# Kernel optimization log

Hardware: AMD Instinct MI355X
Metric: run time of the kernel (lower is better)

## Reference

```python
import jax, jax.numpy as jnp
import numpy as np

B, T, D = 4, 2048, 1024
H = 16            # n_heads
DH = D // H       # head dim
E = 8             # n_micro_experts
DE = 256          # micro_expert_dim
TOP_K = 2
EPS = 1e-5


def _ln(x, g, b):
    m = jnp.mean(x, axis=-1, keepdims=True)
    v = jnp.mean(jnp.square(x - m), axis=-1, keepdims=True)
    return (x - m) * jax.lax.rsqrt(v + EPS) * g + b


def setup_inputs() -> dict:
    key = jax.random.key(0)
    ks = jax.random.split(key, 12)
    s = 0.02
    return {
        "x": jax.random.normal(ks[0], (B, T, D), dtype=jnp.float32),
        "ln1_g": jnp.ones((D,), jnp.float32),
        "ln1_b": jnp.zeros((D,), jnp.float32),
        "in_proj_w": jax.random.normal(ks[1], (3 * D, D), jnp.float32) * s,
        "in_proj_b": jnp.zeros((3 * D,), jnp.float32),
        "out_proj_w": jax.random.normal(ks[2], (D, D), jnp.float32) * s,
        "out_proj_b": jnp.zeros((D,), jnp.float32),
        "ln2_g": jnp.ones((D,), jnp.float32),
        "ln2_b": jnp.zeros((D,), jnp.float32),
        "router_w": jax.random.normal(ks[3], (E, D), jnp.float32) * s,
        "log_temp": jnp.zeros((), jnp.float32),
        "Wg": jax.random.normal(ks[4], (E, DE, D), jnp.float32) * s,  # gate proj per expert
        "Wu": jax.random.normal(ks[5], (E, DE, D), jnp.float32) * s,  # up proj per expert
        "Wd": jax.random.normal(ks[6], (E, D, DE), jnp.float32) * s,  # down proj per expert
    }


def reference(x, ln1_g, ln1_b, in_proj_w, in_proj_b, out_proj_w, out_proj_b,
              ln2_g, ln2_b, router_w, log_temp, Wg, Wu, Wd):
    # --- self-attention block (nn.MultiheadAttention, batch_first, no mask) ---
    h = _ln(x, ln1_g, ln1_b)
    qkv = h @ in_proj_w.T + in_proj_b                       # [B,T,3D]
    q, k, v = jnp.split(qkv, 3, axis=-1)
    q = q.reshape(B, T, H, DH).transpose(0, 2, 1, 3)        # [B,H,T,DH]
    k = k.reshape(B, T, H, DH).transpose(0, 2, 1, 3)
    v = v.reshape(B, T, H, DH).transpose(0, 2, 1, 3)
    scores = jnp.einsum("bhqd,bhkd->bhqk", q, k) / np.sqrt(DH).astype(np.float32)
    attn = jax.nn.softmax(scores, axis=-1)
    o = jnp.einsum("bhqk,bhkd->bhqd", attn, v)              # [B,H,T,DH]
    o = o.transpose(0, 2, 1, 3).reshape(B, T, D)
    x = x + o @ out_proj_w.T + out_proj_b

    # --- MicroExpert MoE (soft top-k via sigmoid suppression, dense experts) ---
    h2 = _ln(x, ln2_g, ln2_b)
    temp = jax.nn.softplus(log_temp) + 0.1
    logits = (h2 @ router_w.T) / temp                       # [B,T,E]
    top_vals, _ = jax.lax.top_k(logits, TOP_K)
    threshold = jax.lax.stop_gradient(top_vals[..., -1:])   # k-th largest, detached
    suppression = jax.nn.sigmoid(10.0 * (logits - threshold))
    weights = jax.nn.softmax(logits * suppression, axis=-1)  # [B,T,E]

    hg = jnp.einsum("btd,efd->btef", h2, Wg)                # [B,T,E,DE]
    hu = jnp.einsum("btd,efd->btef", h2, Wu)
    act = jax.nn.silu(hg) * hu
    out_e = jnp.einsum("btef,edf->bted", act, Wd)           # [B,T,E,D]
    moe = jnp.einsum("bted,bte->btd", out_e, weights)
    return x + moe
```

## Files before the change

### kernel.cpp

```cpp
#include <hip/hip_runtime.h>
#include <hip/hip_bf16.h>
#include <cstddef>
#include <cstdint>

constexpr int Bc  = 4;
constexpr int Tc  = 2048;
constexpr int Dc  = 1024;
constexpr int Hc  = 16;
constexpr int Ec  = 8;
constexpr int DEc = 256;
constexpr int NTOK = Bc * Tc;
constexpr int EDE = Ec * DEc;

typedef __attribute__((ext_vector_type(8)))  short  s8v;
typedef __attribute__((ext_vector_type(4)))  float  f4v;
typedef __attribute__((ext_vector_type(16))) float  f16v;
typedef __attribute__((ext_vector_type(8)))  ushort u8v;
typedef __attribute__((ext_vector_type(4)))  ushort u4v;

constexpr float LOG2E = 1.44269504088896340736f;

__device__ inline ushort f2bf(float f) {
  union { float f; uint32_t u; } v; v.f = f;
  uint32_t r = v.u + 0x7FFFu + ((v.u >> 16) & 1u);
  return (ushort)(r >> 16);
}
__device__ inline float exp2v(float x) {
  float r; asm("v_exp_f32 %0, %1" : "=v"(r) : "v"(x)); return r;
}
__device__ inline float max3f(float a, float b, float c) {
  return fmaxf(fmaxf(a, b), c);
}
__device__ inline float pmax32(float x) {
  float a = x, b = x;
  asm("v_permlane32_swap_b32 %0, %1" : "+v"(b), "+v"(a));
  return fmaxf(a, b);
}
__device__ inline float psum32(float x) {
  float a = x, b = x;
  asm("v_permlane32_swap_b32 %0, %1" : "+v"(b), "+v"(a));
  return a + b;
}

#define GLOAD_LDS(gsrc, ldst)                                        \
  __builtin_amdgcn_global_load_lds(                                  \
      (const __attribute__((address_space(1))) void*)(gsrc),         \
      (__attribute__((address_space(3))) void*)(ldst), 16, 0, 0)

__device__ inline uint32_t cvtpk(float a, float b) {
  uint32_t r;
  asm("v_cvt_pk_bf16_f32 %0, %1, %2" : "=v"(r) : "v"(a), "v"(b));
  return r;
}

__device__ inline u8v pack8(const float4& a, const float4& b) {
  u8v o;
  o[0] = f2bf(a.x); o[1] = f2bf(a.y); o[2] = f2bf(a.z); o[3] = f2bf(a.w);
  o[4] = f2bf(b.x); o[5] = f2bf(b.y); o[6] = f2bf(b.z); o[7] = f2bf(b.w);
  return o;
}

__global__ __launch_bounds__(256)
void convert_all(const float* __restrict__ in_w, const float* __restrict__ out_w,
                 const float* __restrict__ Wg, const float* __restrict__ Wu,
                 const float* __restrict__ Wd,
                 ushort* __restrict__ wb_in, ushort* __restrict__ wb_out,
                 ushort* __restrict__ wb_gu, ushort* __restrict__ wb_d) {
  const int b = blockIdx.x;
  const int tid = threadIdx.x;
  if (b < 1536) {
    const size_t i = ((size_t)b * 256 + tid) * 8;
    *(u8v*)(wb_in + i) = pack8(*(const float4*)(in_w + i),
                               *(const float4*)(in_w + i + 4));
  } else if (b < 2048) {
    const size_t i = ((size_t)(b - 1536) * 256 + tid) * 8;
    *(u8v*)(wb_out + i) = pack8(*(const float4*)(out_w + i),
                                *(const float4*)(out_w + i + 4));
  } else if (b < 4096) {
    const size_t i = ((size_t)(b - 2048) * 256 + tid) * 8;
    const int r = (int)(i >> 10), k = (int)(i & 1023);
    const int j = ((r >> 5) << 4) + (r & 15);
    const float* src = (r & 16) ? Wu : Wg;
    *(u8v*)(wb_gu + i) = pack8(*(const float4*)(src + (size_t)j * Dc + k),
                               *(const float4*)(src + (size_t)j * Dc + k + 4));
  } else {
    const size_t i = ((size_t)(b - 4096) * 256 + tid) * 8;
    const int e = (int)(i >> 18);
    const int d = (int)((i >> 8) & 1023);
    const int f = (int)(i & 255);
    *(u8v*)(wb_d + (size_t)d * EDE + e * DEc + f) =
        pack8(*(const float4*)(Wd + i), *(const float4*)(Wd + i + 4));
  }
}

template <int ROUTER>
__global__ __launch_bounds__(256)
void ln_kernel(const float* __restrict__ in, const float* __restrict__ g,
               const float* __restrict__ bt, ushort* __restrict__ out,
               const float* __restrict__ rw, const float* __restrict__ log_temp,
               float* __restrict__ wts) {
  const int row = blockIdx.x;
  const int tid = threadIdx.x;
  const float* xr = in + (size_t)row * Dc;
  float4 v = *(const float4*)(xr + tid * 4);
  float s  = v.x + v.y + v.z + v.w;
  float ss = v.x * v.x + v.y * v.y + v.z * v.z + v.w * v.w;
#pragma unroll
  for (int off = 32; off; off >>= 1) {
    s  += __shfl_xor(s, off);
    ss += __shfl_xor(ss, off);
  }
  __shared__ float red[8];
  const int w = tid >> 6;
  if ((tid & 63) == 0) { red[w] = s; red[4 + w] = ss; }
  __syncthreads();
  const float ts  = red[0] + red[1] + red[2] + red[3];
  const float tss = red[4] + red[5] + red[6] + red[7];
  const float mean = ts * (1.0f / Dc);
  const float var  = tss * (1.0f / Dc) - mean * mean;
  const float rstd = rsqrtf(var + 1e-5f);
  float4 gv = *(const float4*)(g + tid * 4);
  float4 bv = *(const float4*)(bt + tid * 4);
  const float n0 = (v.x - mean) * rstd * gv.x + bv.x;
  const float n1 = (v.y - mean) * rstd * gv.y + bv.y;
  const float n2 = (v.z - mean) * rstd * gv.z + bv.z;
  const float n3 = (v.w - mean) * rstd * gv.w + bv.w;
  u4v o;
  o[0] = f2bf(n0); o[1] = f2bf(n1); o[2] = f2bf(n2); o[3] = f2bf(n3);
  *(u4v*)(out + (size_t)row * Dc + tid * 4) = o;
  if constexpr (ROUTER) {
    float part[Ec];
#pragma unroll
    for (int e = 0; e < Ec; ++e) {
      float4 wv = *(const float4*)(rw + (size_t)e * Dc + tid * 4);
      part[e] = n0 * wv.x + n1 * wv.y + n2 * wv.z + n3 * wv.w;
    }
#pragma unroll
    for (int off = 32; off; off >>= 1) {
#pragma unroll
      for (int e = 0; e < Ec; ++e) part[e] += __shfl_xor(part[e], off);
    }
    __shared__ float red2[4][Ec];
    if ((tid & 63) == 0) {
#pragma unroll
      for (int e = 0; e < Ec; ++e) red2[w][e] = part[e];
    }
    __syncthreads();
    if (tid == 0) {
      const float lt = *log_temp;
      const float temp = log1pf(__expf(lt)) + 0.1f;
      float lg[Ec];
#pragma unroll
      for (int e = 0; e < Ec; ++e)
        lg[e] = (red2[0][e] + red2[1][e] + red2[2][e] + red2[3][e]) / temp;
      float m1 = -1e30f, m2 = -1e30f;
#pragma unroll
      for (int e = 0; e < Ec; ++e) {
        const float vv = lg[e];
        if (vv > m1) { m2 = m1; m1 = vv; }
        else if (vv > m2) { m2 = vv; }
      }
      float sl[Ec];
      float mx = -1e30f;
#pragma unroll
      for (int e = 0; e < Ec; ++e) {
        const float sup = 1.f / (1.f + __expf(-10.f * (lg[e] - m2)));
        sl[e] = lg[e] * sup;
        mx = fmaxf(mx, sl[e]);
      }
      float ssum = 0.f;
#pragma unroll
      for (int e = 0; e < Ec; ++e) {
        const float p = __expf(sl[e] - mx);
        sl[e] = p;
        ssum += p;
      }
      const float inv = 1.f / ssum;
#pragma unroll
      for (int e = 0; e < Ec; ++e) wts[(size_t)row * Ec + e] = sl[e] * inv;
    }
  }
}

template <int EPI>
__global__ __launch_bounds__(512, 2)
void gemm256(const ushort* __restrict__ A, int lda,
             const ushort* __restrict__ B,
             const float* __restrict__ bias,
             void* __restrict__ Cout, int K) {
  __shared__ __align__(16) ushort Asm[2][256 * 64];
  __shared__ __align__(16) ushort Bsm[2][256 * 64];
  const int tid = threadIdx.x;
  const int lane = tid & 63, w = tid >> 6;
  const int g = lane >> 4, c = lane & 15;
  const int wr = w >> 2, wc = w & 3;
  int bid = blockIdx.y * gridDim.x + blockIdx.x;
  const int qq = (gridDim.x * gridDim.y) >> 3;
  bid = (bid & 7) * qq + (bid >> 3);
  const int m0 = (bid / gridDim.x) * 256, n0 = (bid % gridDim.x) * 256;
  f4v acc[8][4];
#pragma unroll
  for (int i = 0; i < 8; ++i)
#pragma unroll
    for (int j = 0; j < 4; ++j) acc[i][j] = f4v{0.f, 0.f, 0.f, 0.f};

  const int srow = tid >> 3;
  const int koff = 8 * ((tid & 7) ^ (srow & 7));

#define STAGE_A(buf, kt, i)                                                  \
  GLOAD_LDS(A + (size_t)(m0 + (i) * 64 + srow) * lda + (kt) * 64 + koff,     \
            &Asm[buf][((i) * 512 + tid) * 8])
#define STAGE_B(buf, kt, i)                                                  \
  GLOAD_LDS(B + (size_t)(n0 + (i) * 64 + srow) * K + (kt) * 64 + koff,       \
            &Bsm[buf][((i) * 512 + tid) * 8])

#define RD_A(buf, mi, ks)                                                    \
  (*(const s8v*)&Asm[buf][(wr * 128 + (mi) * 16 + c) * 64 +                  \
      8 * (((ks) * 4 + g) ^ ((wr * 128 + (mi) * 16 + c) & 7))])
#define RD_B(buf, ni, ks)                                                    \
  (*(const s8v*)&Bsm[buf][(wc * 64 + (ni) * 16 + c) * 64 +                   \
      8 * (((ks) * 4 + g) ^ ((wc * 64 + (ni) * 16 + c) & 7))])

  const int NT = K >> 6;
  STAGE_B(0, 0, 0); STAGE_B(0, 0, 1); STAGE_B(0, 0, 2); STAGE_B(0, 0, 3);
  STAGE_A(0, 0, 0); STAGE_A(0, 0, 2); STAGE_A(0, 0, 1); STAGE_A(0, 0, 3);
  asm volatile("s_waitcnt vmcnt(0)" ::: "memory");
  __builtin_amdgcn_s_barrier();

  for (int t = 0; t < NT; ++t) {
    const int cur = t & 1, nxt = cur ^ 1;
    const bool st = (t + 1 < NT);
    s8v bf[2][4], af[2][2];
#pragma unroll
    for (int ks = 0; ks < 2; ++ks) {
#pragma unroll
      for (int ni = 0; ni < 4; ++ni) bf[ks][ni] = RD_B(cur, ni, ks);
      af[ks][0] = RD_A(cur, 0, ks); af[ks][1] = RD_A(cur, 1, ks);
    }
    if (st) { STAGE_B(nxt, t + 1, 0); STAGE_B(nxt, t + 1, 1); }
    __builtin_amdgcn_s_barrier();
    __builtin_amdgcn_s_setprio(1);
#pragma unroll
    for (int ks = 0; ks < 2; ++ks)
#pragma unroll
      for (int q = 0; q < 2; ++q)
#pragma unroll
        for (int ni = 0; ni < 4; ++ni)
          acc[q][ni] = __builtin_amdgcn_mfma_f32_16x16x32_bf16(
              af[ks][q], bf[ks][ni], acc[q][ni], 0, 0, 0);
    __builtin_amdgcn_s_setprio(0);
    __builtin_amdgcn_s_barrier();
#pragma unroll
    for (int ks = 0; ks < 2; ++ks) {
      af[ks][0] = RD_A(cur, 2, ks); af[ks][1] = RD_A(cur, 3, ks);
    }
    if (st) { STAGE_B(nxt, t + 1, 2); STAGE_B(nxt, t + 1, 3); }
    __builtin_amdgcn_s_barrier();
    __builtin_amdgcn_s_setprio(1);
#pragma unroll
    for (int ks = 0; ks < 2; ++ks)
#pragma unroll
      for (int q = 0; q < 2; ++q)
#pragma unroll
        for (int ni = 0; ni < 4; ++ni)
          acc[2 + q][ni] = __builtin_amdgcn_mfma_f32_16x16x32_bf16(
              af[ks][q], bf[ks][ni], acc[2 + q][ni], 0, 0, 0);
    __builtin_amdgcn_s_setprio(0);
    if (st) asm volatile("s_waitcnt vmcnt(4)" ::: "memory");
    else    asm volatile("s_waitcnt vmcnt(0)" ::: "memory");
    __builtin_amdgcn_s_barrier();
#pragma unroll
    for (int ks = 0; ks < 2; ++ks) {
      af[ks][0] = RD_A(cur, 4, ks); af[ks][1] = RD_A(cur, 5, ks);
    }
    if (st) { STAGE_A(nxt, t + 1, 0); STAGE_A(nxt, t + 1, 2); }
    __builtin_amdgcn_s_barrier();
    __builtin_amdgcn_s_setprio(1);
#pragma unroll
    for (int ks = 0; ks < 2; ++ks)
#pragma unroll
      for (int q = 0; q < 2; ++q)
#pragma unroll
        for (int ni = 0; ni < 4; ++ni)
          acc[4 + q][ni] = __builtin_amdgcn_mfma_f32_16x16x32_bf16(
              af[ks][q], bf[ks][ni], acc[4 + q][ni], 0, 0, 0);
    __builtin_amdgcn_s_setprio(0);
    __builtin_amdgcn_s_barrier();
#pragma unroll
    for (int ks = 0; ks < 2; ++ks) {
      af[ks][0] = RD_A(cur, 6, ks); af[ks][1] = RD_A(cur, 7, ks);
    }
    if (st) { STAGE_A(nxt, t + 1, 1); STAGE_A(nxt, t + 1, 3); }
    __builtin_amdgcn_s_barrier();
    __builtin_amdgcn_s_setprio(1);
#pragma unroll
    for (int ks = 0; ks < 2; ++ks)
#pragma unroll
      for (int q = 0; q < 2; ++q)
#pragma unroll
        for (int ni = 0; ni < 4; ++ni)
          acc[6 + q][ni] = __builtin_amdgcn_mfma_f32_16x16x32_bf16(
              af[ks][q], bf[ks][ni], acc[6 + q][ni], 0, 0, 0);
    __builtin_amdgcn_s_setprio(0);
    if (st) asm volatile("s_waitcnt vmcnt(2)" ::: "memory");
    __builtin_amdgcn_s_barrier();
  }
#undef STAGE_A
#undef STAGE_B
#undef RD_A
#undef RD_B

#pragma unroll
  for (int mi = 0; mi < 8; ++mi) {
    if constexpr (EPI == 4) {
#pragma unroll
      for (int nip = 0; nip < 2; ++nip) {
        const int jbase = ((n0 + wc * 64) >> 1) + nip * 16;
        const int e = jbase >> 8;
#pragma unroll
        for (int j = 0; j < 4; ++j) {
          const int row = m0 + wr * 128 + mi * 16 + g * 4 + j;
          const float wgt = bias[(size_t)row * Ec + e];
          const float gv = acc[mi][2 * nip][j];
          const float uv = acc[mi][2 * nip + 1][j];
          const float av = (gv / (1.f + __expf(-gv))) * uv * wgt;
          ((ushort*)Cout)[(size_t)row * EDE + jbase + c] = f2bf(av);
        }
      }
    } else {
#pragma unroll
      for (int ni = 0; ni < 4; ++ni) {
        const int col = n0 + wc * 64 + ni * 16 + c;
        const int which = col >> 10, hh = (col >> 6) & 15, d = col & 63;
        const int row0 = m0 + wr * 128 + mi * 16 + g * 4;
        const int b = row0 >> 11, t0 = row0 & 2047;
        const float bs = bias[col];
        ushort* base = (ushort*)Cout;
        if (which == 2) {
          u4v pk;
#pragma unroll
          for (int j = 0; j < 4; ++j) pk[j] = f2bf(acc[mi][ni][j] + bs);
          *(u4v*)&base[2 * (size_t)NTOK * Dc +
                       (((size_t)(b * Hc + hh)) * 64 + d) * Tc + t0] = pk;
        } else {
          const float qs = (which == 0) ? 0.125f * LOG2E : 1.f;
          const size_t off = (size_t)which * ((size_t)NTOK * Dc);
#pragma unroll
          for (int j = 0; j < 4; ++j)
            base[off + (((size_t)(b * Hc + hh)) * Tc + t0 + j) * 64 + d] =
                f2bf((acc[mi][ni][j] + bs) * qs);
        }
      }
    }
  }
}

template <int EPI>
__global__ __launch_bounds__(256)
void gemm_bf16(const ushort* __restrict__ A, int lda,
               const ushort* __restrict__ B,
               const float* __restrict__ bias, const float* __restrict__ resid,
               void* __restrict__ Cout, int ldc, int K) {
  __shared__ __align__(16) ushort As[128 * 32];
  __shared__ __align__(16) ushort Bs[128 * 32];
  const int tid = threadIdx.x;
  const int lane = tid & 63, w = tid >> 6;
  const int g = lane >> 4, c = lane & 15;
  int bid = blockIdx.y * gridDim.x + blockIdx.x;
  const int qq = (gridDim.x * gridDim.y) >> 3;
  bid = (bid & 7) * qq + (bid >> 3);
  const int m0 = (bid / gridDim.x) * 128, n0 = (bid % gridDim.x) * 128;
  const int wm = (w >> 1) * 64, wn = (w & 1) * 64;
  f4v acc[4][4];
#pragma unroll
  for (int i = 0; i < 4; ++i)
#pragma unroll
    for (int j = 0; j < 4; ++j) acc[i][j] = f4v{0.f, 0.f, 0.f, 0.f};

  int srow[2], skoff[2];
#pragma unroll
  for (int seg = 0; seg < 2; ++seg) {
    const int ci = seg * 256 + tid;
    srow[seg] = ci >> 2;
    skoff[seg] = 8 * ((ci & 3) ^ ((srow[seg] >> 1) & 3));
  }

  for (int k0 = 0; k0 < K; k0 += 32) {
#pragma unroll
    for (int seg = 0; seg < 2; ++seg) {
      const int ci = seg * 256 + tid;
      GLOAD_LDS(A + (size_t)(m0 + srow[seg]) * lda + k0 + skoff[seg], &As[ci * 8]);
      GLOAD_LDS(B + (size_t)(n0 + srow[seg]) * K + k0 + skoff[seg], &Bs[ci * 8]);
    }
    __syncthreads();
    s8v af[4], bf[4];
#pragma unroll
    for (int mi = 0; mi < 4; ++mi) {
      const int R = wm + mi * 16 + c;
      af[mi] = *(const s8v*)&As[R * 32 + 8 * (g ^ ((R >> 1) & 3))];
    }
#pragma unroll
    for (int ni = 0; ni < 4; ++ni) {
      const int R = wn + ni * 16 + c;
      bf[ni] = *(const s8v*)&Bs[R * 32 + 8 * (g ^ ((R >> 1) & 3))];
    }
#pragma unroll
    for (int mi = 0; mi < 4; ++mi)
#pragma unroll
      for (int ni = 0; ni < 4; ++ni)
        acc[mi][ni] = __builtin_amdgcn_mfma_f32_16x16x32_bf16(
            af[mi], bf[ni], acc[mi][ni], 0, 0, 0);
    __syncthreads();
  }

#pragma unroll
  for (int mi = 0; mi < 4; ++mi) {
#pragma unroll
    for (int ni = 0; ni < 4; ++ni) {
#pragma unroll
      for (int j = 0; j < 4; ++j) {
        const int row = m0 + wm + mi * 16 + g * 4 + j;
        const int col = n0 + wn + ni * 16 + c;
        float v = acc[mi][ni][j];
        if constexpr (EPI == 1) {
          v += bias[col] + resid[(size_t)row * ldc + col];
          ((float*)Cout)[(size_t)row * ldc + col] = v;
        } else {
          ((float*)Cout)[(size_t)row * ldc + col] += v;
        }
      }
    }
  }
}

__global__ __launch_bounds__(256)
void attn_mfma(const ushort* __restrict__ Qb, const ushort* __restrict__ Kb,
               const ushort* __restrict__ Vt, ushort* __restrict__ Ob) {
  __shared__ __align__(16) ushort Ksm[2][64 * 64];
  __shared__ __align__(16) ushort Vtsm[2][64 * 64];
  const int tid = threadIdx.x;
  const int lane = tid & 63, w = tid >> 6;
  const int ql = lane & 31, hi = lane >> 5;
  int bid = blockIdx.x;
  bid = (bid & 7) * 128 + (bid >> 3);
  const int qt = bid & 15, bh = bid >> 4;
  const ushort* Qh = Qb + (size_t)bh * Tc * 64;
  const ushort* Kh = Kb + (size_t)bh * Tc * 64;
  const ushort* Vth = Vt + (size_t)bh * 64 * Tc;
  const int qrow = qt * 128 + w * 32 + ql;
  s8v qf[4];
#pragma unroll
  for (int ds = 0; ds < 4; ++ds)
    qf[ds] = *(const s8v*)(Qh + (size_t)qrow * 64 + ds * 16 + hi * 8);
  f16v accO0, accO1;
#pragma unroll
  for (int i = 0; i < 16; ++i) { accO0[i] = 0.f; accO1[i] = 0.f; }
  float mold = -1e30f, lsum = 0.f;
  int srow[2], soff[2];
#pragma unroll
  for (int seg = 0; seg < 2; ++seg) {
    const int ci = seg * 256 + tid;
    srow[seg] = ci >> 3;
    soff[seg] = ((ci & 7) * 8) ^ ((srow[seg] & 7) << 3);
  }
  auto stage = [&](int buf, int j0) {
#pragma unroll
    for (int seg = 0; seg < 2; ++seg) {
      const int ci = seg * 256 + tid;
      GLOAD_LDS(Kh + (size_t)(j0 + srow[seg]) * 64 + soff[seg], &Ksm[buf][ci * 8]);
      GLOAD_LDS(Vth + (size_t)srow[seg] * Tc + j0 + soff[seg], &Vtsm[buf][ci * 8]);
    }
  };

  stage(0, 0);
  int cur = 0;
  for (int j0 = 0; j0 < Tc; j0 += 64) {
    const bool st = (j0 + 64 < Tc);
    if (st) {
      stage(cur ^ 1, j0 + 64);
      asm volatile("s_waitcnt vmcnt(4)" ::: "memory");
    } else {
      asm volatile("s_waitcnt vmcnt(0)" ::: "memory");
    }
    __builtin_amdgcn_s_barrier();
    f16v s0, s1;
#pragma unroll
    for (int i = 0; i < 16; ++i) { s0[i] = 0.f; s1[i] = 0.f; }
    __builtin_amdgcn_s_setprio(1);
#pragma unroll
    for (int ds = 0; ds < 4; ++ds) {
      const int col = (ds * 16 + hi * 8);
      const int r0 = ql;
      s8v kf0 = *(const s8v*)&Ksm[cur][r0 * 64 + (col ^ ((r0 & 7) << 3))];
      s0 = __builtin_amdgcn_mfma_f32_32x32x16_bf16(kf0, qf[ds], s0, 0, 0, 0);
      const int r1 = 32 + ql;
      s8v kf1 = *(const s8v*)&Ksm[cur][r1 * 64 + (col ^ ((r1 & 7) << 3))];
      s1 = __builtin_amdgcn_mfma_f32_32x32x16_bf16(kf1, qf[ds], s1, 0, 0, 0);
    }
    __builtin_amdgcn_s_setprio(0);
    float cc0 = fmaxf(s0[0], s1[0]), cc1 = fmaxf(s0[1], s1[1]);
    float cc2 = fmaxf(s0[2], s1[2]), cc3 = fmaxf(s0[3], s1[3]);
#pragma unroll
    for (int i = 4; i < 16; i += 4) {
      cc0 = max3f(cc0, s0[i + 0], s1[i + 0]);
      cc1 = max3f(cc1, s0[i + 1], s1[i + 1]);
      cc2 = max3f(cc2, s0[i + 2], s1[i + 2]);
      cc3 = max3f(cc3, s0[i + 3], s1[i + 3]);
    }
    float mx = pmax32(fmaxf(max3f(cc0, cc1, cc2), cc3));
    const bool need = mx > mold + 11.5416f;
    if (__any((int)need)) {
      const float mnew = fmaxf(mold, mx);
      const float sc = exp2v(mold - mnew);
      lsum *= sc;
#pragma unroll
      for (int i = 0; i < 16; ++i) { accO0[i] *= sc; accO1[i] *= sc; }
      mold = mnew;
    }
    float r0s = 0.f, r1s = 0.f, r2s = 0.f, r3s = 0.f;
#pragma unroll
    for (int i = 0; i < 16; i += 4) {
      s0[i+0] = exp2v(s0[i+0] - mold); r0s += s0[i+0];
      s0[i+1] = exp2v(s0[i+1] - mold); r1s += s0[i+1];
      s0[i+2] = exp2v(s0[i+2] - mold); r2s += s0[i+2];
      s0[i+3] = exp2v(s0[i+3] - mold); r3s += s0[i+3];
      s1[i+0] = exp2v(s1[i+0] - mold); r0s += s1[i+0];
      s1[i+1] = exp2v(s1[i+1] - mold); r1s += s1[i+1];
      s1[i+2] = exp2v(s1[i+2] - mold); r2s += s1[i+2];
      s1[i+3] = exp2v(s1[i+3] - mold); r3s += s1[i+3];
    }
    lsum += psum32((r0s + r1s) + (r2s + r3s));
    s8v pa[4];
#pragma unroll
    for (int s = 0; s < 4; ++s) {
      const f16v st2 = (s < 2) ? s0 : s1;
      const int mA = 2 * (s & 1);
      uint32_t a0 = cvtpk(st2[4 * mA + 0], st2[4 * mA + 1]);
      uint32_t a1 = cvtpk(st2[4 * mA + 2], st2[4 * mA + 3]);
      uint32_t b0 = cvtpk(st2[4 * mA + 4], st2[4 * mA + 5]);
      uint32_t b1 = cvtpk(st2[4 * mA + 6], st2[4 * mA + 7]);
      asm("v_permlane32_swap_b32 %0, %1" : "+v"(b0), "+v"(a0));
      asm("v_permlane32_swap_b32 %0, %1" : "+v"(b1), "+v"(a1));
      union { uint32_t u[4]; s8v v; } pk;
      pk.u[0] = a0; pk.u[1] = a1; pk.u[2] = b0; pk.u[3] = b1;
      pa[s] = pk.v;
    }
    __builtin_amdgcn_s_setprio(1);
#pragma unroll
    for (int s = 0; s < 4; ++s) {
      const int col = (s * 16 + hi * 8);
      const int r0 = ql;
      s8v vf0 = *(const s8v*)&Vtsm[cur][r0 * 64 + (col ^ ((r0 & 7) << 3))];
      accO0 = __builtin_amdgcn_mfma_f32_32x32x16_bf16(vf0, pa[s], accO0, 0, 0, 0);
      const int r1 = 32 + ql;
      s8v vf1 = *(const s8v*)&Vtsm[cur][r1 * 64 + (col ^ ((r1 & 7) << 3))];
      accO1 = __builtin_amdgcn_mfma_f32_32x32x16_bf16(vf1, pa[s], accO1, 0, 0, 0);
    }
    __builtin_amdgcn_s_setprio(0);
    __builtin_amdgcn_s_barrier();
    cur ^= 1;
  }
  const int h = bh & 15, b = bh >> 4;
  const int tok = b * Tc + qt * 128 + w * 32 + ql;
  const float inv = 1.f / lsum;
  ushort* orow = Ob + (size_t)tok * Dc + h * 64;
#pragma unroll
  for (int dt = 0; dt < 2; ++dt) {
    const f16v ac = dt ? accO1 : accO0;
#pragma unroll
    for (int rq = 0; rq < 4; ++rq) {
      u4v pk;
#pragma unroll
      for (int j = 0; j < 4; ++j) pk[j] = f2bf(ac[4 * rq + j] * inv);
      *(u4v*)&orow[dt * 32 + 8 * rq + 4 * hi] = pk;
    }
  }
}

extern "C" void kernel_launch(void* const* d_in, const int* in_sizes, int n_in,
                              void* d_out, int out_size, void* d_ws, size_t ws_size,
                              hipStream_t stream) {
  (void)in_sizes; (void)n_in; (void)out_size; (void)ws_size;
  const float* x        = (const float*)d_in[0];
  const float* ln1_g    = (const float*)d_in[1];
  const float* ln1_b    = (const float*)d_in[2];
  const float* in_w     = (const float*)d_in[3];
  const float* in_b     = (const float*)d_in[4];
  const float* out_w    = (const float*)d_in[5];
  const float* out_b    = (const float*)d_in[6];
  const float* ln2_g    = (const float*)d_in[7];
  const float* ln2_b    = (const float*)d_in[8];
  const float* rw       = (const float*)d_in[9];
  const float* log_temp = (const float*)d_in[10];
  const float* Wg       = (const float*)d_in[11];
  const float* Wu       = (const float*)d_in[12];
  const float* Wd       = (const float*)d_in[13];
  float* out = (float*)d_out;

  ushort* h_bf   = (ushort*)d_ws;
  ushort* Qb     = h_bf   + (size_t)NTOK * Dc;
  ushort* Kb     = Qb     + (size_t)NTOK * Dc;
  ushort* Vt     = Kb     + (size_t)NTOK * Dc;
  ushort* Ob     = Vt     + (size_t)NTOK * Dc;
  ushort* act    = Ob     + (size_t)NTOK * Dc;
  ushort* wb_in  = act    + (size_t)NTOK * EDE;
  ushort* wb_out = wb_in  + (size_t)3 * Dc * Dc;
  ushort* wb_gu  = wb_out + (size_t)Dc * Dc;
  ushort* wb_d   = wb_gu  + (size_t)2 * EDE * Dc;
  float*  wts    = (float*)(wb_d + (size_t)Dc * EDE);

  const dim3 blk(256);

  convert_all<<<dim3(5120), blk, 0, stream>>>(
      in_w, out_w, Wg, Wu, Wd, wb_in, wb_out, wb_gu, wb_d);

  ln_kernel<0><<<dim3(NTOK), blk, 0, stream>>>(x, ln1_g, ln1_b, h_bf,
                                               nullptr, nullptr, nullptr);
  gemm256<0><<<dim3(3 * Dc / 256, NTOK / 256), dim3(512), 0, stream>>>(
      h_bf, Dc, wb_in, in_b, Qb, Dc);
  attn_mfma<<<dim3(Bc * Hc * (Tc / 128)), blk, 0, stream>>>(Qb, Kb, Vt, Ob);
  gemm_bf16<1><<<dim3(Dc / 128, NTOK / 128), blk, 0, stream>>>(
      Ob, Dc, wb_out, out_b, x, out, Dc, Dc);
  ln_kernel<1><<<dim3(NTOK), blk, 0, stream>>>(out, ln2_g, ln2_b, h_bf,
                                               rw, log_temp, wts);
  gemm256<4><<<dim3(2 * EDE / 256, NTOK / 256), dim3(512), 0, stream>>>(
      h_bf, Dc, wb_gu, wts, act, Dc);
  gemm_bf16<3><<<dim3(Dc / 128, NTOK / 128), blk, 0, stream>>>(
      act, EDE, wb_d, nullptr, nullptr, out, Dc, EDE);
}
```

Measured before the change: 404.8 us.

## Double-buffer LDS tiles in bf16 GEMM to overlap global loads with MFMA

The generic bf16 GEMM now keeps two LDS buffers per operand and issues the global-to-LDS loads for the next K step before computing on the current one. It waits on outstanding loads with an explicit vmcnt count instead of a full sync, so load latency is meant to be hidden behind the MFMA work. It also raises wave priority around the MFMA block. LDS use per block doubles, which may lower occupancy, and correctness depends on the hand-written vmcnt(4) matching the four loads issued per stage.

```diff
diff --git a/kernel.cpp b/kernel.cpp
--- a/kernel.cpp
+++ b/kernel.cpp
@@ -361,8 +361,8 @@
                const ushort* __restrict__ B,
                const float* __restrict__ bias, const float* __restrict__ resid,
                void* __restrict__ Cout, int ldc, int K) {
-  __shared__ __align__(16) ushort As[128 * 32];
-  __shared__ __align__(16) ushort Bs[128 * 32];
+  __shared__ __align__(16) ushort As[2][128 * 32];
+  __shared__ __align__(16) ushort Bs[2][128 * 32];
   const int tid = threadIdx.x;
   const int lane = tid & 63, w = tid >> 6;
   const int g = lane >> 4, c = lane & 15;
@@ -384,33 +384,49 @@
     srow[seg] = ci >> 2;
     skoff[seg] = 8 * ((ci & 3) ^ ((srow[seg] >> 1) & 3));
   }
-
-  for (int k0 = 0; k0 < K; k0 += 32) {
+  auto stage = [&](int buf, int k0) {
 #pragma unroll
     for (int seg = 0; seg < 2; ++seg) {
       const int ci = seg * 256 + tid;
-      GLOAD_LDS(A + (size_t)(m0 + srow[seg]) * lda + k0 + skoff[seg], &As[ci * 8]);
-      GLOAD_LDS(B + (size_t)(n0 + srow[seg]) * K + k0 + skoff[seg], &Bs[ci * 8]);
-    }
-    __syncthreads();
+      GLOAD_LDS(A + (size_t)(m0 + srow[seg]) * lda + k0 + skoff[seg],
+                &As[buf][ci * 8]);
+      GLOAD_LDS(B + (size_t)(n0 + srow[seg]) * K + k0 + skoff[seg],
+                &Bs[buf][ci * 8]);
+    }
+  };
+
+  stage(0, 0);
+  int curb = 0;
+  for (int k0 = 0; k0 < K; k0 += 32) {
+    const bool st = (k0 + 32 < K);
+    if (st) {
+      stage(curb ^ 1, k0 + 32);
+      asm volatile("s_waitcnt vmcnt(4)" ::: "memory");
+    } else {
+      asm volatile("s_waitcnt vmcnt(0)" ::: "memory");
+    }
+    __builtin_amdgcn_s_barrier();
     s8v af[4], bf[4];
 #pragma unroll
     for (int mi = 0; mi < 4; ++mi) {
       const int R = wm + mi * 16 + c;
-      af[mi] = *(const s8v*)&As[R * 32 + 8 * (g ^ ((R >> 1) & 3))];
+      af[mi] = *(const s8v*)&As[curb][R * 32 + 8 * (g ^ ((R >> 1) & 3))];
     }
 #pragma unroll
     for (int ni = 0; ni < 4; ++ni) {
       const int R = wn + ni * 16 + c;
-      bf[ni] = *(const s8v*)&Bs[R * 32 + 8 * (g ^ ((R >> 1) & 3))];
-    }
+      bf[ni] = *(const s8v*)&Bs[curb][R * 32 + 8 * (g ^ ((R >> 1) & 3))];
+    }
+    __builtin_amdgcn_s_setprio(1);
 #pragma unroll
     for (int mi = 0; mi < 4; ++mi)
 #pragma unroll
       for (int ni = 0; ni < 4; ++ni)
         acc[mi][ni] = __builtin_amdgcn_mfma_f32_16x16x32_bf16(
             af[mi], bf[ni], acc[mi][ni], 0, 0, 0);
-    __syncthreads();
+    __builtin_amdgcn_s_setprio(0);
+    __builtin_amdgcn_s_barrier();
+    curb ^= 1;
   }
 
 #pragma unroll
```

Result: no change. 402.9 us (-0.5%).
